# Optimization experiments

Measured on AMD Instinct MI355X. Metric: run time of the kernel, lower is better.

The kernel has to match this reference:

```python
import jax, jax.numpy as jnp
import numpy as np

C64 = jnp.complex64
N_WIRES = 4


def _rx_b(theta):  # theta: [b] -> [b,2,2]
    c = jnp.cos(theta / 2).astype(C64)
    s = (-1j * jnp.sin(theta / 2)).astype(C64)
    return jnp.stack([jnp.stack([c, s], -1), jnp.stack([s, c], -1)], -2)


def _ry_b(theta):
    c = jnp.cos(theta / 2).astype(C64)
    s = jnp.sin(theta / 2).astype(C64)
    return jnp.stack([jnp.stack([c, -s], -1), jnp.stack([s, c], -1)], -2)


def _rz_b(theta):
    em = jnp.exp(-1j * theta.astype(C64) / 2)
    ep = jnp.exp(1j * theta.astype(C64) / 2)
    z = jnp.zeros_like(em)
    return jnp.stack([jnp.stack([em, z], -1), jnp.stack([z, ep], -1)], -2)


def _crx_mat(theta):  # scalar -> [4,4]
    c = jnp.cos(theta / 2).astype(C64)
    s = (-1j * jnp.sin(theta / 2)).astype(C64)
    m = jnp.eye(4, dtype=C64)
    m = m.at[2, 2].set(c).at[3, 3].set(c).at[2, 3].set(s).at[3, 2].set(s)
    return m


def _apply_1q(state, U, w):
    # state: [b,2,2,2,2]; U: [b,2,2] (batched) or [2,2]
    s = jnp.moveaxis(state, w + 1, 1)
    sh = s.shape
    s = s.reshape(sh[0], 2, -1)
    if U.ndim == 3:
        s = jnp.einsum('bij,bjr->bir', U, s)
    else:
        s = jnp.einsum('ij,bjr->bir', U, s)
    return jnp.moveaxis(s.reshape(sh), 1, w + 1)


def _apply_2q(state, U, wa, wb):
    # state: [b,2,2,2,2]; U: [4,4]; wa = first wire (high bit of U index)
    s = jnp.moveaxis(state, (wa + 1, wb + 1), (1, 2))
    sh = s.shape
    s = s.reshape(sh[0], 4, -1)
    s = jnp.einsum('ij,bjr->bir', U, s)
    return jnp.moveaxis(s.reshape(sh), (1, 2), (wa + 1, wb + 1))


_H = (1.0 / np.sqrt(2.0)) * jnp.array([[1, 1], [1, -1]], dtype=C64)
_SX = 0.5 * jnp.array([[1 + 1j, 1 - 1j], [1 - 1j, 1 + 1j]], dtype=C64)
_CNOT = jnp.array([[1, 0, 0, 0], [0, 1, 0, 0], [0, 0, 0, 1], [0, 0, 1, 0]], dtype=C64)
_U12 = jnp.array([[1, 0, 0, 0], [0, 1, 0, 0], [0, 0, 0, 1j], [0, 0, -1j, 0]], dtype=C64)


def setup_inputs() -> dict:
    key = jax.random.key(0)
    k0, k1, k2, k3, k4 = jax.random.split(key, 5)
    bsz = 131072
    return {
        'x': jax.random.normal(k0, (bsz, 1, 24, 24), dtype=jnp.float32),
        'theta_rx0': jax.random.normal(k1, (1,), dtype=jnp.float32),
        'theta_ry0': jax.random.normal(k2, (1,), dtype=jnp.float32),
        'theta_rz0': jax.random.normal(k3, (1,), dtype=jnp.float32),
        'theta_crx0': jax.random.normal(k4, (1,), dtype=jnp.float32),
    }


def reference(x, theta_rx0, theta_ry0, theta_rz0, theta_crx0):
    b = x.shape[0]
    # avg_pool2d(kernel=6, stride=6) on 24x24 -> 4x4, flatten to 16 angles
    xp = x.reshape(b, 4, 6, 4, 6).mean(axis=(2, 4)).reshape(b, 16)
    # |0000> state
    state = jnp.zeros((b, 2, 2, 2, 2), dtype=C64).at[:, 0, 0, 0, 0].set(1.0)
    # encoder: rx*4, ry*4, rz*4, rx*4 on wires k % 4 with batched angles
    for k in range(4):
        state = _apply_1q(state, _rx_b(xp[:, k]), k)
    for k in range(4):
        state = _apply_1q(state, _ry_b(xp[:, 4 + k]), k)
    for k in range(4):
        state = _apply_1q(state, _rz_b(xp[:, 8 + k]), k)
    for k in range(4):
        state = _apply_1q(state, _rx_b(xp[:, 12 + k]), k)
    # trainable gates (shared scalar params)
    state = _apply_1q(state, _rx_b(theta_rx0)[0], 0)
    state = _apply_1q(state, _ry_b(theta_ry0)[0], 1)
    state = _apply_1q(state, _rz_b(theta_rz0)[0], 3)
    state = _apply_2q(state, _crx_mat(theta_crx0[0]), 0, 2)
    state = _apply_1q(state, _H, 3)
    state = _apply_1q(state, _SX, 2)
    state = _apply_2q(state, _CNOT, 3, 0)
    state = _apply_2q(state, _U12, 1, 2)
    # MeasureAll(PauliZ): <Z_w> per wire
    probs = state.real ** 2 + state.imag ** 2  # [b,2,2,2,2]
    zvals = jnp.array([1.0, -1.0], dtype=probs.dtype)
    exps = []
    for w in range(N_WIRES):
        shape = [1] + [2 if i == w else 1 for i in range(N_WIRES)]
        exps.append((probs * zvals.reshape(shape)).sum(axis=(1, 2, 3, 4)))
    z = jnp.stack(exps, axis=-1)  # [b,4]
    logits = z.reshape(b, 2, 2).sum(-1)  # [b,2]
    return jax.nn.log_softmax(logits, axis=1)
```

## Files before the change

### kernel.cpp

```cpp
#include <hip/hip_runtime.h>


#define CH 8
#define PADF 584
#define XPS 132
#define NCHUNK 16

__device__ __forceinline__ void cmul(float ar, float ai, float br, float bi,
                                     float& cr, float& ci) {
  cr = ar * br - ai * bi;
  ci = ar * bi + ai * br;
}

struct C2 { float r0, i0, r1, i1; };

__device__ __forceinline__ void g_rx(C2& v, float h) {
  float s, c; __sincosf(h, &s, &c);
  C2 n;
  n.r0 = c * v.r0 + s * v.i1;
  n.i0 = c * v.i0 - s * v.r1;
  n.r1 = c * v.r1 + s * v.i0;
  n.i1 = c * v.i1 - s * v.r0;
  v = n;
}
__device__ __forceinline__ void g_ry(C2& v, float h) {
  float s, c; __sincosf(h, &s, &c);
  C2 n;
  n.r0 = c * v.r0 - s * v.r1;
  n.i0 = c * v.i0 - s * v.i1;
  n.r1 = s * v.r0 + c * v.r1;
  n.i1 = s * v.i0 + c * v.i1;
  v = n;
}
__device__ __forceinline__ void g_rz(C2& v, float h) {
  float s, c; __sincosf(h, &s, &c);
  C2 n;
  n.r0 = c * v.r0 + s * v.i0;
  n.i0 = c * v.i0 - s * v.r0;
  n.r1 = c * v.r1 - s * v.i1;
  n.i1 = c * v.i1 + s * v.r1;
  v = n;
}

__global__ __launch_bounds__(256, 3)
void qfc_kernel(const float* __restrict__ x,
                const float* __restrict__ thrx,
                const float* __restrict__ thry,
                const float* __restrict__ thrz,
                const float* __restrict__ thcrx,
                float* __restrict__ out) {
  __shared__ float stage[2][CH * PADF];
  __shared__ float xp[16][XPS];

  const int t = threadIdx.x;
  const long long img0 = (long long)blockIdx.x * 128;
  const float4* __restrict__ x4 = reinterpret_cast<const float4*>(x);

  float4 s0, s1, s2, s3, s4;

  auto load_chunk = [&](int c) {
    long long base = (img0 + (long long)c * CH) * 144;
    s0 = x4[base + (0 * 256 + t)];
    s1 = x4[base + (1 * 256 + t)];
    s2 = x4[base + (2 * 256 + t)];
    s3 = x4[base + (3 * 256 + t)];
    if (t < 128) s4 = x4[base + (4 * 256 + t)];
  };
  auto write_chunk = [&](int buf) {
    float* sp = stage[buf];
    auto wr = [&](int idx, float4 v) {
      int img = idx / 144;
      int off4 = idx - img * 144;
      *reinterpret_cast<float4*>(&sp[img * PADF + off4 * 4]) = v;
    };
    wr(0 * 256 + t, s0);
    wr(1 * 256 + t, s1);
    wr(2 * 256 + t, s2);
    wr(3 * 256 + t, s3);
    if (t < 128) wr(4 * 256 + t, s4);
  };

  load_chunk(0);
  write_chunk(0);
  __syncthreads();

  for (int c = 0; c < NCHUNK; ++c) {
    if (c + 1 < NCHUNK) load_chunk(c + 1);
    if (t < CH * 16) {
      int img = t >> 4;
      int pool = t & 15;
      int r0 = pool >> 2, c0 = pool & 3;
      const float* b = &stage[c & 1][img * PADF + r0 * 144 + c0 * 6];
      float sum = 0.f;
#pragma unroll
      for (int r = 0; r < 6; ++r) {
        float2 a0 = *reinterpret_cast<const float2*>(b + r * 24);
        float2 a1 = *reinterpret_cast<const float2*>(b + r * 24 + 2);
        float2 a2 = *reinterpret_cast<const float2*>(b + r * 24 + 4);
        sum += a0.x + a0.y + a1.x + a1.y + a2.x + a2.y;
      }
      xp[pool][c * CH + img] = sum * (1.0f / 36.0f);
    }
    __syncthreads();
    if (c + 1 < NCHUNK) write_chunk((c + 1) & 1);
    __syncthreads();
  }

  if (t < 128) {
    float a[16];
#pragma unroll
    for (int j = 0; j < 16; ++j) a[j] = xp[j][t];

    const float arx = thrx[0] * 0.5f;
    const float ary = thry[0] * 0.5f;
    const float arz = thrz[0] * 0.5f;
    const float acr = thcrx[0] * 0.5f;

    C2 v[4];
#pragma unroll
    for (int w = 0; w < 4; ++w) {
      v[w].r0 = 1.f; v[w].i0 = 0.f; v[w].r1 = 0.f; v[w].i1 = 0.f;
      g_rx(v[w], a[w] * 0.5f);
      g_ry(v[w], a[4 + w] * 0.5f);
      g_rz(v[w], a[8 + w] * 0.5f);
      g_rx(v[w], a[12 + w] * 0.5f);
    }
    g_rx(v[0], arx);
    g_ry(v[1], ary);
    g_rz(v[3], arz);

    float t01r[4], t01i[4], t23r[4], t23i[4];
    cmul(v[0].r0, v[0].i0, v[1].r0, v[1].i0, t01r[0], t01i[0]);
    cmul(v[0].r0, v[0].i0, v[1].r1, v[1].i1, t01r[1], t01i[1]);
    cmul(v[0].r1, v[0].i1, v[1].r0, v[1].i0, t01r[2], t01i[2]);
    cmul(v[0].r1, v[0].i1, v[1].r1, v[1].i1, t01r[3], t01i[3]);
    cmul(v[2].r0, v[2].i0, v[3].r0, v[3].i0, t23r[0], t23i[0]);
    cmul(v[2].r0, v[2].i0, v[3].r1, v[3].i1, t23r[1], t23i[1]);
    cmul(v[2].r1, v[2].i1, v[3].r0, v[3].i0, t23r[2], t23i[2]);
    cmul(v[2].r1, v[2].i1, v[3].r1, v[3].i1, t23r[3], t23i[3]);

    float re[16], im[16];
#pragma unroll
    for (int hi = 0; hi < 4; ++hi)
#pragma unroll
      for (int lo = 0; lo < 4; ++lo)
        cmul(t01r[hi], t01i[hi], t23r[lo], t23i[lo], re[hi * 4 + lo], im[hi * 4 + lo]);

    {
      float s, cc2; __sincosf(acr, &s, &cc2);
#pragma unroll
      for (int k = 0; k < 4; ++k) {
        const int pi4[4] = {8, 9, 12, 13};
        int i = pi4[k], j = i + 2;
        float nir = cc2 * re[i] + s * im[j];
        float nii = cc2 * im[i] - s * re[j];
        float njr = cc2 * re[j] + s * im[i];
        float nji = cc2 * im[j] - s * re[i];
        re[i] = nir; im[i] = nii; re[j] = njr; im[j] = nji;
      }
    }
#pragma unroll
    for (int i = 0; i < 16; i += 2) {
      const float inv = 0.70710678118654752f;
      float ar = re[i], ai = im[i], br = re[i + 1], bi = im[i + 1];
      re[i] = (ar + br) * inv;     im[i] = (ai + bi) * inv;
      re[i + 1] = (ar - br) * inv; im[i + 1] = (ai - bi) * inv;
    }
#pragma unroll
    for (int i = 0; i < 16; ++i) {
      if ((i & 2) == 0) {
        int j = i + 2;
        float ar = re[i], ai = im[i], br = re[j], bi = im[j];
        re[i] = 0.5f * (ar - ai + br + bi);
        im[i] = 0.5f * (ar + ai - br + bi);
        re[j] = 0.5f * (ar + ai + br - bi);
        im[j] = 0.5f * (ai - ar + br + bi);
      }
    }
#pragma unroll
    for (int i = 1; i < 8; i += 2) {
      float tr = re[i], ti = im[i];
      re[i] = re[i + 8]; im[i] = im[i + 8];
      re[i + 8] = tr;    im[i + 8] = ti;
    }
#pragma unroll
    for (int k = 0; k < 4; ++k) {
      const int ii4[4] = {4, 5, 12, 13};
      int i = ii4[k], j = i + 2;
      float tr = re[i], ti = im[i];
      re[i] = -im[j]; im[i] = re[j];
      re[j] = ti;     im[j] = -tr;
    }

    float z0 = 0.f, z1 = 0.f, z2 = 0.f, z3 = 0.f;
#pragma unroll
    for (int i = 0; i < 16; ++i) {
      float p = re[i] * re[i] + im[i] * im[i];
      z0 += (i & 8) ? -p : p;
      z1 += (i & 4) ? -p : p;
      z2 += (i & 2) ? -p : p;
      z3 += (i & 1) ? -p : p;
    }
    float l0 = z0 + z1, l1 = z2 + z3;
    float m = fmaxf(l0, l1);
    float e0 = __expf(l0 - m), e1 = __expf(l1 - m);
    float lse = __logf(e0 + e1);
    float2 o;
    o.x = l0 - m - lse;
    o.y = l1 - m - lse;
    reinterpret_cast<float2*>(out)[img0 + t] = o;
  }
}

extern "C" void kernel_launch(void* const* d_in, const int* in_sizes, int n_in,
                              void* d_out, int out_size, void* d_ws, size_t ws_size,
                              hipStream_t stream) {
  const float* x = (const float*)d_in[0];
  const float* thrx = (const float*)d_in[1];
  const float* thry = (const float*)d_in[2];
  const float* thrz = (const float*)d_in[3];
  const float* thcrx = (const float*)d_in[4];
  float* out = (float*)d_out;
  qfc_kernel<<<1024, 256, 0, stream>>>(x, thrx, thry, thrz, thcrx, out);
}
```

Measured before the change: 56.52 us.

## Triple-buffer LDS staging with two register chunks in flight, 256 images per block

The pooling stage moves from a double-buffered LDS ring with one register prefetch to a triple-buffered ring that keeps two chunks of global loads in flight in registers (rA/rB). This removes one barrier per chunk, since writes to buffer c+1 no longer have to wait for all pooling of c. Each block now handles 256 images in 32 chunks with all 256 threads running the quantum-circuit epilogue, and the grid is halved to 512 blocks. The cost is more LDS per block (about 56KB) and more registers, so launch bounds drop to 2 blocks per CU. That lowers occupancy and leaves fewer blocks in flight for a memory-bound kernel.

```diff
diff --git a/kernel.cpp b/kernel.cpp
--- a/kernel.cpp
+++ b/kernel.cpp
@@ -3,8 +3,9 @@
 
 #define CH 8
 #define PADF 584
-#define XPS 132
-#define NCHUNK 16
+#define BUF_F (CH * PADF)
+#define XPS 257
+#define NCHUNK 32
 
 __device__ __forceinline__ void cmul(float ar, float ai, float br, float bi,
                                      float& cr, float& ci) {
@@ -42,55 +43,49 @@
   v = n;
 }
 
-__global__ __launch_bounds__(256, 3)
+__global__ __launch_bounds__(256, 2)
 void qfc_kernel(const float* __restrict__ x,
                 const float* __restrict__ thrx,
                 const float* __restrict__ thry,
                 const float* __restrict__ thrz,
                 const float* __restrict__ thcrx,
                 float* __restrict__ out) {
-  __shared__ float stage[2][CH * PADF];
-  __shared__ float xp[16][XPS];
+  __shared__ float stage[3 * BUF_F];
+  __shared__ float xp[16 * XPS];
 
   const int t = threadIdx.x;
-  const long long img0 = (long long)blockIdx.x * 128;
+  const long long img0 = (long long)blockIdx.x * 256;
   const float4* __restrict__ x4 = reinterpret_cast<const float4*>(x);
 
-  float4 s0, s1, s2, s3, s4;
-
-  auto load_chunk = [&](int c) {
+  float4 rA[5], rB[5];
+
+  auto issue = [&](float4* r, int c) {
     long long base = (img0 + (long long)c * CH) * 144;
-    s0 = x4[base + (0 * 256 + t)];
-    s1 = x4[base + (1 * 256 + t)];
-    s2 = x4[base + (2 * 256 + t)];
-    s3 = x4[base + (3 * 256 + t)];
-    if (t < 128) s4 = x4[base + (4 * 256 + t)];
+    r[0] = x4[base + (0 * 256 + t)];
+    r[1] = x4[base + (1 * 256 + t)];
+    r[2] = x4[base + (2 * 256 + t)];
+    r[3] = x4[base + (3 * 256 + t)];
+    if (t < 128) r[4] = x4[base + (4 * 256 + t)];
   };
-  auto write_chunk = [&](int buf) {
-    float* sp = stage[buf];
+  auto put = [&](const float4* r, int buf) {
+    float* sp = stage + buf * BUF_F;
     auto wr = [&](int idx, float4 v) {
       int img = idx / 144;
       int off4 = idx - img * 144;
       *reinterpret_cast<float4*>(&sp[img * PADF + off4 * 4]) = v;
     };
-    wr(0 * 256 + t, s0);
-    wr(1 * 256 + t, s1);
-    wr(2 * 256 + t, s2);
-    wr(3 * 256 + t, s3);
-    if (t < 128) wr(4 * 256 + t, s4);
+    wr(0 * 256 + t, r[0]);
+    wr(1 * 256 + t, r[1]);
+    wr(2 * 256 + t, r[2]);
+    wr(3 * 256 + t, r[3]);
+    if (t < 128) wr(4 * 256 + t, r[4]);
   };
-
-  load_chunk(0);
-  write_chunk(0);
-  __syncthreads();
-
-  for (int c = 0; c < NCHUNK; ++c) {
-    if (c + 1 < NCHUNK) load_chunk(c + 1);
-    if (t < CH * 16) {
+  auto pool = [&](int c, int buf) {
+    if (t < 128) {
       int img = t >> 4;
-      int pool = t & 15;
-      int r0 = pool >> 2, c0 = pool & 3;
-      const float* b = &stage[c & 1][img * PADF + r0 * 144 + c0 * 6];
+      int p = t & 15;
+      int r0 = p >> 2, c0 = p & 3;
+      const float* b = &stage[buf * BUF_F + img * PADF + r0 * 144 + c0 * 6];
       float sum = 0.f;
 #pragma unroll
       for (int r = 0; r < 6; ++r) {
@@ -99,117 +94,136 @@
         float2 a2 = *reinterpret_cast<const float2*>(b + r * 24 + 4);
         sum += a0.x + a0.y + a1.x + a1.y + a2.x + a2.y;
       }
-      xp[pool][c * CH + img] = sum * (1.0f / 36.0f);
+      xp[p * XPS + c * CH + img] = sum * (1.0f / 36.0f);
     }
+  };
+
+  issue(rA, 0);
+  issue(rB, 1);
+  put(rA, 0);
+  __syncthreads();
+  issue(rA, 2);
+  pool(0, 0);
+
+  for (int p = 0; p < 15; ++p) {
+    const int c1 = 2 * p + 1;
+    const int c2 = 2 * p + 2;
+    put(rB, c1 % 3);
     __syncthreads();
-    if (c + 1 < NCHUNK) write_chunk((c + 1) & 1);
+    if (c1 + 2 < NCHUNK) issue(rB, c1 + 2);
+    pool(c1, c1 % 3);
+    put(rA, c2 % 3);
     __syncthreads();
-  }
-
-  if (t < 128) {
-    float a[16];
-#pragma unroll
-    for (int j = 0; j < 16; ++j) a[j] = xp[j][t];
-
-    const float arx = thrx[0] * 0.5f;
-    const float ary = thry[0] * 0.5f;
-    const float arz = thrz[0] * 0.5f;
-    const float acr = thcrx[0] * 0.5f;
-
-    C2 v[4];
-#pragma unroll
-    for (int w = 0; w < 4; ++w) {
-      v[w].r0 = 1.f; v[w].i0 = 0.f; v[w].r1 = 0.f; v[w].i1 = 0.f;
-      g_rx(v[w], a[w] * 0.5f);
-      g_ry(v[w], a[4 + w] * 0.5f);
-      g_rz(v[w], a[8 + w] * 0.5f);
-      g_rx(v[w], a[12 + w] * 0.5f);
+    if (c2 + 2 < NCHUNK) issue(rA, c2 + 2);
+    pool(c2, c2 % 3);
+  }
+  put(rB, 31 % 3);
+  __syncthreads();
+  pool(31, 31 % 3);
+  __syncthreads();
+
+  float a[16];
+#pragma unroll
+  for (int j = 0; j < 16; ++j) a[j] = xp[j * XPS + t];
+
+  const float arx = thrx[0] * 0.5f;
+  const float ary = thry[0] * 0.5f;
+  const float arz = thrz[0] * 0.5f;
+  const float acr = thcrx[0] * 0.5f;
+
+  C2 v[4];
+#pragma unroll
+  for (int w = 0; w < 4; ++w) {
+    v[w].r0 = 1.f; v[w].i0 = 0.f; v[w].r1 = 0.f; v[w].i1 = 0.f;
+    g_rx(v[w], a[w] * 0.5f);
+    g_ry(v[w], a[4 + w] * 0.5f);
+    g_rz(v[w], a[8 + w] * 0.5f);
+    g_rx(v[w], a[12 + w] * 0.5f);
+  }
+  g_rx(v[0], arx);
+  g_ry(v[1], ary);
+  g_rz(v[3], arz);
+
+  float t01r[4], t01i[4], t23r[4], t23i[4];
+  cmul(v[0].r0, v[0].i0, v[1].r0, v[1].i0, t01r[0], t01i[0]);
+  cmul(v[0].r0, v[0].i0, v[1].r1, v[1].i1, t01r[1], t01i[1]);
+  cmul(v[0].r1, v[0].i1, v[1].r0, v[1].i0, t01r[2], t01i[2]);
+  cmul(v[0].r1, v[0].i1, v[1].r1, v[1].i1, t01r[3], t01i[3]);
+  cmul(v[2].r0, v[2].i0, v[3].r0, v[3].i0, t23r[0], t23i[0]);
+  cmul(v[2].r0, v[2].i0, v[3].r1, v[3].i1, t23r[1], t23i[1]);
+  cmul(v[2].r1, v[2].i1, v[3].r0, v[3].i0, t23r[2], t23i[2]);
+  cmul(v[2].r1, v[2].i1, v[3].r1, v[3].i1, t23r[3], t23i[3]);
+
+  float re[16], im[16];
+#pragma unroll
+  for (int hi = 0; hi < 4; ++hi)
+#pragma unroll
+    for (int lo = 0; lo < 4; ++lo)
+      cmul(t01r[hi], t01i[hi], t23r[lo], t23i[lo], re[hi * 4 + lo], im[hi * 4 + lo]);
+
+  {
+    float s, cc2; __sincosf(acr, &s, &cc2);
+#pragma unroll
+    for (int k = 0; k < 4; ++k) {
+      const int pi4[4] = {8, 9, 12, 13};
+      int i = pi4[k], j = i + 2;
+      float nir = cc2 * re[i] + s * im[j];
+      float nii = cc2 * im[i] - s * re[j];
+      float njr = cc2 * re[j] + s * im[i];
+      float nji = cc2 * im[j] - s * re[i];
+      re[i] = nir; im[i] = nii; re[j] = njr; im[j] = nji;
     }
-    g_rx(v[0], arx);
-    g_ry(v[1], ary);
-    g_rz(v[3], arz);
-
-    float t01r[4], t01i[4], t23r[4], t23i[4];
-    cmul(v[0].r0, v[0].i0, v[1].r0, v[1].i0, t01r[0], t01i[0]);
-    cmul(v[0].r0, v[0].i0, v[1].r1, v[1].i1, t01r[1], t01i[1]);
-    cmul(v[0].r1, v[0].i1, v[1].r0, v[1].i0, t01r[2], t01i[2]);
-    cmul(v[0].r1, v[0].i1, v[1].r1, v[1].i1, t01r[3], t01i[3]);
-    cmul(v[2].r0, v[2].i0, v[3].r0, v[3].i0, t23r[0], t23i[0]);
-    cmul(v[2].r0, v[2].i0, v[3].r1, v[3].i1, t23r[1], t23i[1]);
-    cmul(v[2].r1, v[2].i1, v[3].r0, v[3].i0, t23r[2], t23i[2]);
-    cmul(v[2].r1, v[2].i1, v[3].r1, v[3].i1, t23r[3], t23i[3]);
-
-    float re[16], im[16];
-#pragma unroll
-    for (int hi = 0; hi < 4; ++hi)
-#pragma unroll
-      for (int lo = 0; lo < 4; ++lo)
-        cmul(t01r[hi], t01i[hi], t23r[lo], t23i[lo], re[hi * 4 + lo], im[hi * 4 + lo]);
-
-    {
-      float s, cc2; __sincosf(acr, &s, &cc2);
-#pragma unroll
-      for (int k = 0; k < 4; ++k) {
-        const int pi4[4] = {8, 9, 12, 13};
-        int i = pi4[k], j = i + 2;
-        float nir = cc2 * re[i] + s * im[j];
-        float nii = cc2 * im[i] - s * re[j];
-        float njr = cc2 * re[j] + s * im[i];
-        float nji = cc2 * im[j] - s * re[i];
-        re[i] = nir; im[i] = nii; re[j] = njr; im[j] = nji;
-      }
+  }
+#pragma unroll
+  for (int i = 0; i < 16; i += 2) {
+    const float inv = 0.70710678118654752f;
+    float ar = re[i], ai = im[i], br = re[i + 1], bi = im[i + 1];
+    re[i] = (ar + br) * inv;     im[i] = (ai + bi) * inv;
+    re[i + 1] = (ar - br) * inv; im[i + 1] = (ai - bi) * inv;
+  }
+#pragma unroll
+  for (int i = 0; i < 16; ++i) {
+    if ((i & 2) == 0) {
+      int j = i + 2;
+      float ar = re[i], ai = im[i], br = re[j], bi = im[j];
+      re[i] = 0.5f * (ar - ai + br + bi);
+      im[i] = 0.5f * (ar + ai - br + bi);
+      re[j] = 0.5f * (ar + ai + br - bi);
+      im[j] = 0.5f * (ai - ar + br + bi);
     }
-#pragma unroll
-    for (int i = 0; i < 16; i += 2) {
-      const float inv = 0.70710678118654752f;
-      float ar = re[i], ai = im[i], br = re[i + 1], bi = im[i + 1];
-      re[i] = (ar + br) * inv;     im[i] = (ai + bi) * inv;
-      re[i + 1] = (ar - br) * inv; im[i + 1] = (ai - bi) * inv;
-    }
-#pragma unroll
-    for (int i = 0; i < 16; ++i) {
-      if ((i & 2) == 0) {
-        int j = i + 2;
-        float ar = re[i], ai = im[i], br = re[j], bi = im[j];
-        re[i] = 0.5f * (ar - ai + br + bi);
-        im[i] = 0.5f * (ar + ai - br + bi);
-        re[j] = 0.5f * (ar + ai + br - bi);
-        im[j] = 0.5f * (ai - ar + br + bi);
-      }
-    }
-#pragma unroll
-    for (int i = 1; i < 8; i += 2) {
-      float tr = re[i], ti = im[i];
-      re[i] = re[i + 8]; im[i] = im[i + 8];
-      re[i + 8] = tr;    im[i + 8] = ti;
-    }
-#pragma unroll
-    for (int k = 0; k < 4; ++k) {
-      const int ii4[4] = {4, 5, 12, 13};
-      int i = ii4[k], j = i + 2;
-      float tr = re[i], ti = im[i];
-      re[i] = -im[j]; im[i] = re[j];
-      re[j] = ti;     im[j] = -tr;
-    }
-
-    float z0 = 0.f, z1 = 0.f, z2 = 0.f, z3 = 0.f;
-#pragma unroll
-    for (int i = 0; i < 16; ++i) {
-      float p = re[i] * re[i] + im[i] * im[i];
-      z0 += (i & 8) ? -p : p;
-      z1 += (i & 4) ? -p : p;
-      z2 += (i & 2) ? -p : p;
-      z3 += (i & 1) ? -p : p;
-    }
-    float l0 = z0 + z1, l1 = z2 + z3;
-    float m = fmaxf(l0, l1);
-    float e0 = __expf(l0 - m), e1 = __expf(l1 - m);
-    float lse = __logf(e0 + e1);
-    float2 o;
-    o.x = l0 - m - lse;
-    o.y = l1 - m - lse;
-    reinterpret_cast<float2*>(out)[img0 + t] = o;
-  }
+  }
+#pragma unroll
+  for (int i = 1; i < 8; i += 2) {
+    float tr = re[i], ti = im[i];
+    re[i] = re[i + 8]; im[i] = im[i + 8];
+    re[i + 8] = tr;    im[i + 8] = ti;
+  }
+#pragma unroll
+  for (int k = 0; k < 4; ++k) {
+    const int ii4[4] = {4, 5, 12, 13};
+    int i = ii4[k], j = i + 2;
+    float tr = re[i], ti = im[i];
+    re[i] = -im[j]; im[i] = re[j];
+    re[j] = ti;     im[j] = -tr;
+  }
+
+  float z0 = 0.f, z1 = 0.f, z2 = 0.f, z3 = 0.f;
+#pragma unroll
+  for (int i = 0; i < 16; ++i) {
+    float p = re[i] * re[i] + im[i] * im[i];
+    z0 += (i & 8) ? -p : p;
+    z1 += (i & 4) ? -p : p;
+    z2 += (i & 2) ? -p : p;
+    z3 += (i & 1) ? -p : p;
+  }
+  float l0 = z0 + z1, l1 = z2 + z3;
+  float m = fmaxf(l0, l1);
+  float e0 = __expf(l0 - m), e1 = __expf(l1 - m);
+  float lse = __logf(e0 + e1);
+  float2 o;
+  o.x = l0 - m - lse;
+  o.y = l1 - m - lse;
+  reinterpret_cast<float2*>(out)[img0 + t] = o;
 }
 
 extern "C" void kernel_launch(void* const* d_in, const int* in_sizes, int n_in,
@@ -221,5 +235,5 @@
   const float* thrz = (const float*)d_in[3];
   const float* thcrx = (const float*)d_in[4];
   float* out = (float*)d_out;
-  qfc_kernel<<<1024, 256, 0, stream>>>(x, thrx, thry, thrz, thcrx, out);
-}
+  qfc_kernel<<<512, 256, 0, stream>>>(x, thrx, thry, thrz, thcrx, out);
+}
```

Result: faster. 52.24 us (-7.6%).
